# Kernel optimization log

Hardware: AMD Instinct MI355X
Metric: run time of the kernel (lower is better)

The kernel has to match this reference:

```python
import jax, jax.numpy as jnp
import numpy as np

B, C, H, D, HID = 1024, 64, 64, 256, 256

def setup_inputs() -> dict:
    key = jax.random.key(0)
    k1, k2, k3, k4, k5, k6, k7, k8 = jax.random.split(key, 8)
    candidate_news_vector = jax.random.normal(k1, (B, C, D), dtype=jnp.float32)
    clicked_news_vector = jax.random.normal(k2, (B, H, D), dtype=jnp.float32)
    mask_cand = jax.random.randint(k3, (B, C), 0, 2).astype(bool).at[:, 0].set(True)
    mask_hist = jax.random.randint(k4, (B, H), 0, 2).astype(bool).at[:, 0].set(True)
    # nn.Linear default init: U(-1/sqrt(fan_in), 1/sqrt(fan_in))
    s1 = 1.0 / np.sqrt(2 * D)
    s2 = 1.0 / np.sqrt(HID)
    W1 = jax.random.uniform(k5, (HID, 2 * D), minval=-s1, maxval=s1, dtype=jnp.float32)
    b1 = jax.random.uniform(k6, (HID,), minval=-s1, maxval=s1, dtype=jnp.float32)
    W2 = jax.random.uniform(k7, (1, HID), minval=-s2, maxval=s2, dtype=jnp.float32)
    b2 = jax.random.uniform(k8, (1,), minval=-s2, maxval=s2, dtype=jnp.float32)
    return {"candidate_news_vector": candidate_news_vector,
            "clicked_news_vector": clicked_news_vector,
            "mask_cand": mask_cand, "mask_hist": mask_hist,
            "W1": W1, "b1": b1, "W2": W2, "b2": b2}

def reference(candidate_news_vector, clicked_news_vector, mask_cand, mask_hist, W1, b1, W2, b2):
    d = candidate_news_vector.shape[-1]
    w2 = W2[0]                                  # [HID]
    # Two stacked Linears with no nonlinearity collapse exactly:
    # score = (W2 @ W1_c) . cand + (W2 @ W1_h) . hist + (W2 @ b1 + b2)
    v_c = W1[:, :d].T @ w2                      # [D]
    v_h = W1[:, d:].T @ w2                      # [D]
    bias = jnp.dot(w2, b1) + b2[0]
    scores = (jnp.einsum('bcd,d->bc', candidate_news_vector, v_c)[:, :, None]
              + jnp.einsum('bhd,d->bh', clicked_news_vector, v_h)[:, None, :]
              + bias)                           # [B, C, H]
    neg = jnp.finfo(scores.dtype).min
    scores = jnp.where(mask_hist[:, None, :], scores, neg)
    weights = jax.nn.softmax(scores, axis=-1)   # [B, C, H]
    weights = jnp.where(mask_cand[:, :, None], weights, 0.0)
    user_vector = jnp.einsum('bch,bhd->bcd', weights, clicked_news_vector)
    return user_vector
```

## Files before the change

kernel.cpp:

```cpp
#include <hip/hip_runtime.h>
#include <math.h>

#define NB 1024
#define NC 64
#define NH 64
#define ND 256
#define NHID 256

typedef float f4 __attribute__((ext_vector_type(4)));

#define WS_PART_OFF 1024

__device__ __forceinline__ bool read_mask(const void* m, int idx, int mode) {
  if (mode == 2) return ((const float*)m)[idx] != 0.0f;
  if (mode == 1) return ((const unsigned char*)m)[idx] != 0;
  return ((const int*)m)[idx] != 0;
}

__device__ __forceinline__ void detect_mode(const unsigned int* mask_cand,
                                            const unsigned int* mask_hist,
                                            int* dst) {
  int sawf = 0; unsigned int big = 0;
  for (int i = 0; i < 32; ++i) {
    unsigned int a = mask_hist[i], b = mask_cand[i];
    if (a == 0x3f800000u || b == 0x3f800000u) sawf = 1;
    if ((a > 1u && a != 0x3f800000u) || (b > 1u && b != 0x3f800000u)) big = 1;
  }
  *dst = sawf ? 2 : (big ? 1 : 0);
}

__device__ __forceinline__ float dot4(f4 a, f4 b) {
  return fmaf(a.x, b.x, fmaf(a.y, b.y, fmaf(a.z, b.z, a.w * b.w)));
}

#define BFLY(p) { p += __shfl_xor(p, 32); p += __shfl_xor(p, 16); p += __shfl_xor(p, 8); \
                  p += __shfl_xor(p, 4);  p += __shfl_xor(p, 2);  p += __shfl_xor(p, 1); }

__global__ __launch_bounds__(256) void precompute_p1(
    const float* __restrict__ W1, const float* __restrict__ W2,
    float* __restrict__ ws)
{
  const int g = blockIdx.x;
  const int d = threadIdx.x;
  float acc = 0.f;
  #pragma unroll
  for (int jj = 0; jj < 4; ++jj) {
    int j = g * 4 + jj;
    acc = fmaf(W1[(size_t)j * (2 * ND) + ND + d], W2[j], acc);
  }
  ws[WS_PART_OFF + g * ND + d] = acc;
}

__global__ __launch_bounds__(256) void precompute_p2(
    const unsigned int* __restrict__ mask_cand,
    const unsigned int* __restrict__ mask_hist,
    float* __restrict__ ws)
{
  const int d = threadIdx.x;
  float acc = 0.f;
  #pragma unroll 8
  for (int g = 0; g < 64; ++g) acc += ws[WS_PART_OFF + g * ND + d];
  ws[d] = acc;
  if (d == 0) detect_mode(mask_cand, mask_hist, (int*)ws + ND);
}

__global__ __launch_bounds__(1024) void precompute_fallback(
    const float* __restrict__ W1, const float* __restrict__ W2,
    const unsigned int* __restrict__ mask_cand,
    const unsigned int* __restrict__ mask_hist,
    float* __restrict__ ws)
{
  __shared__ float w2_lds[NHID];
  __shared__ float partial[4][ND];
  int t = threadIdx.x;
  if (t < NHID) w2_lds[t] = W2[t];
  __syncthreads();
  int d = t & (ND - 1);
  int g = t >> 8;
  float acc = 0.f;
  #pragma unroll 8
  for (int j = g * 64; j < g * 64 + 64; ++j)
    acc = fmaf(W1[(size_t)j * (2 * ND) + ND + d], w2_lds[j], acc);
  partial[g][d] = acc;
  __syncthreads();
  if (t < ND)
    ws[t] = partial[0][t] + partial[1][t] + partial[2][t] + partial[3][t];
  if (t == 0) detect_mode(mask_cand, mask_hist, (int*)ws + ND);
}

__global__ __launch_bounds__(512, 8) void fused_kernel(
    const float* __restrict__ hist,
    const void* __restrict__ mask_cand_v,
    const void* __restrict__ mask_hist_v,
    const float* __restrict__ ws,
    float* __restrict__ out)
{
  const int b = blockIdx.x, t = threadIdx.x, lane = t & 63, w = t >> 6;
  __shared__ float s_lds[NH];
  __shared__ f4 red[8][64];

  const int mode = ((const int*)ws)[ND];
  const f4* hb4 = reinterpret_cast<const f4*>(hist) + (size_t)b * 4096;
  const f4 vh = reinterpret_cast<const f4*>(ws)[lane];

  bool mc[8];
  #pragma unroll
  for (int j = 0; j < 8; ++j)
    mc[j] = read_mask(mask_cand_v, b * NC + w * 8 + j, mode);

  f4 x0 = hb4[(w * 8 + 0) * 64 + lane], x1 = hb4[(w * 8 + 1) * 64 + lane];
  f4 x2 = hb4[(w * 8 + 2) * 64 + lane], x3 = hb4[(w * 8 + 3) * 64 + lane];
  f4 x4 = hb4[(w * 8 + 4) * 64 + lane], x5 = hb4[(w * 8 + 5) * 64 + lane];
  f4 x6 = hb4[(w * 8 + 6) * 64 + lane], x7 = hb4[(w * 8 + 7) * 64 + lane];

  float p0 = dot4(x0, vh), p1 = dot4(x1, vh), p2 = dot4(x2, vh), p3 = dot4(x3, vh);
  float p4 = dot4(x4, vh), p5 = dot4(x5, vh), p6 = dot4(x6, vh), p7 = dot4(x7, vh);
  BFLY(p0) BFLY(p1) BFLY(p2) BFLY(p3) BFLY(p4) BFLY(p5) BFLY(p6) BFLY(p7)

  if (lane < 8) {
    float v = p0;
    if (lane == 1) v = p1;  if (lane == 2) v = p2;  if (lane == 3) v = p3;
    if (lane == 4) v = p4;  if (lane == 5) v = p5;  if (lane == 6) v = p6;
    if (lane == 7) v = p7;
    int h = w * 8 + lane;
    s_lds[h] = read_mask(mask_hist_v, b * NH + h, mode) ? v : -3.0e38f;
  }
  __syncthreads();

  float wval;
  {
    float s = s_lds[lane];
    float m = s;
    m = fmaxf(m, __shfl_xor(m, 32)); m = fmaxf(m, __shfl_xor(m, 16));
    m = fmaxf(m, __shfl_xor(m, 8));  m = fmaxf(m, __shfl_xor(m, 4));
    m = fmaxf(m, __shfl_xor(m, 2));  m = fmaxf(m, __shfl_xor(m, 1));
    float e = expf(s - m);
    float sum = e;
    BFLY(sum)
    wval = e / sum;
  }

  {
    f4 acc = __shfl(wval, w * 8 + 0) * x0;
    acc += __shfl(wval, w * 8 + 1) * x1;
    acc += __shfl(wval, w * 8 + 2) * x2;
    acc += __shfl(wval, w * 8 + 3) * x3;
    acc += __shfl(wval, w * 8 + 4) * x4;
    acc += __shfl(wval, w * 8 + 5) * x5;
    acc += __shfl(wval, w * 8 + 6) * x6;
    acc += __shfl(wval, w * 8 + 7) * x7;
    red[w][lane] = acc;
  }
  __syncthreads();

  f4 uv = red[0][lane];
  #pragma unroll
  for (int q = 1; q < 8; ++q) uv += red[q][lane];

  f4* ob4 = reinterpret_cast<f4*>(out) + (size_t)b * 4096;
  const f4 zero = {0.f, 0.f, 0.f, 0.f};
  #pragma unroll
  for (int j = 0; j < 8; ++j) {
    int c = w * 8 + j;
    ob4[c * 64 + lane] = mc[j] ? uv : zero;
  }
}

extern "C" void kernel_launch(void* const* d_in, const int* in_sizes, int n_in,
                              void* d_out, int out_size, void* d_ws, size_t ws_size,
                              hipStream_t stream) {
  (void)in_sizes; (void)n_in; (void)out_size;
  const float* hist = (const float*)d_in[1];
  const void*  mask_cand = d_in[2];
  const void*  mask_hist = d_in[3];
  const float* W1 = (const float*)d_in[4];
  const float* W2 = (const float*)d_in[6];
  float* ws = (float*)d_ws;
  float* out = (float*)d_out;

  if (ws_size >= (size_t)(WS_PART_OFF + 64 * ND) * sizeof(float)) {
    precompute_p1<<<64, 256, 0, stream>>>(W1, W2, ws);
    precompute_p2<<<1, 256, 0, stream>>>(
        (const unsigned int*)mask_cand, (const unsigned int*)mask_hist, ws);
  } else {
    precompute_fallback<<<1, 1024, 0, stream>>>(
        W1, W2, (const unsigned int*)mask_cand, (const unsigned int*)mask_hist, ws);
  }
  fused_kernel<<<NB, 512, 0, stream>>>(hist, mask_cand, mask_hist, ws, out);
}
```

Measured before the change: 43.46 us.

## Process two batches per block and prefetch the second batch's history during the first

The fused kernel now handles two batch rows per block, launching half as many blocks. The second row's history tile is loaded while the first row's weighted sum and output write proceed, so memory latency overlaps with compute. This doubles the register footprint, lowers the occupancy hint, and halves the number of blocks available to fill the GPU.

New measurement: 40.34 us. -7.2%, faster.

```diff
diff --git a/kernel.cpp b/kernel.cpp
--- a/kernel.cpp
+++ b/kernel.cpp
@@ -88,81 +88,135 @@
   if (t == 0) detect_mode(mask_cand, mask_hist, (int*)ws + ND);
 }
 
-__global__ __launch_bounds__(512, 8) void fused_kernel(
+__global__ __launch_bounds__(512, 4) void fused2_kernel(
     const float* __restrict__ hist,
     const void* __restrict__ mask_cand_v,
     const void* __restrict__ mask_hist_v,
     const float* __restrict__ ws,
     float* __restrict__ out)
 {
-  const int b = blockIdx.x, t = threadIdx.x, lane = t & 63, w = t >> 6;
-  __shared__ float s_lds[NH];
-  __shared__ f4 red[8][64];
+  const int b0 = blockIdx.x, b1 = blockIdx.x + 512;
+  const int t = threadIdx.x, lane = t & 63, w = t >> 6;
+  __shared__ float s_lds[2][NH];
+  __shared__ f4 red[2][8][64];
 
   const int mode = ((const int*)ws)[ND];
-  const f4* hb4 = reinterpret_cast<const f4*>(hist) + (size_t)b * 4096;
   const f4 vh = reinterpret_cast<const f4*>(ws)[lane];
-
-  bool mc[8];
-  #pragma unroll
-  for (int j = 0; j < 8; ++j)
-    mc[j] = read_mask(mask_cand_v, b * NC + w * 8 + j, mode);
-
-  f4 x0 = hb4[(w * 8 + 0) * 64 + lane], x1 = hb4[(w * 8 + 1) * 64 + lane];
-  f4 x2 = hb4[(w * 8 + 2) * 64 + lane], x3 = hb4[(w * 8 + 3) * 64 + lane];
-  f4 x4 = hb4[(w * 8 + 4) * 64 + lane], x5 = hb4[(w * 8 + 5) * 64 + lane];
-  f4 x6 = hb4[(w * 8 + 6) * 64 + lane], x7 = hb4[(w * 8 + 7) * 64 + lane];
+  const f4* h0 = reinterpret_cast<const f4*>(hist) + (size_t)b0 * 4096;
+  const f4* h1 = reinterpret_cast<const f4*>(hist) + (size_t)b1 * 4096;
+  const f4 zero = {0.f, 0.f, 0.f, 0.f};
+
+  f4 x0 = h0[(w * 8 + 0) * 64 + lane], x1 = h0[(w * 8 + 1) * 64 + lane];
+  f4 x2 = h0[(w * 8 + 2) * 64 + lane], x3 = h0[(w * 8 + 3) * 64 + lane];
+  f4 x4 = h0[(w * 8 + 4) * 64 + lane], x5 = h0[(w * 8 + 5) * 64 + lane];
+  f4 x6 = h0[(w * 8 + 6) * 64 + lane], x7 = h0[(w * 8 + 7) * 64 + lane];
 
   float p0 = dot4(x0, vh), p1 = dot4(x1, vh), p2 = dot4(x2, vh), p3 = dot4(x3, vh);
   float p4 = dot4(x4, vh), p5 = dot4(x5, vh), p6 = dot4(x6, vh), p7 = dot4(x7, vh);
   BFLY(p0) BFLY(p1) BFLY(p2) BFLY(p3) BFLY(p4) BFLY(p5) BFLY(p6) BFLY(p7)
-
   if (lane < 8) {
     float v = p0;
     if (lane == 1) v = p1;  if (lane == 2) v = p2;  if (lane == 3) v = p3;
     if (lane == 4) v = p4;  if (lane == 5) v = p5;  if (lane == 6) v = p6;
     if (lane == 7) v = p7;
     int h = w * 8 + lane;
-    s_lds[h] = read_mask(mask_hist_v, b * NH + h, mode) ? v : -3.0e38f;
-  }
-  __syncthreads();
-
-  float wval;
-  {
-    float s = s_lds[lane];
+    s_lds[0][h] = read_mask(mask_hist_v, b0 * NH + h, mode) ? v : -3.0e38f;
+  }
+  __syncthreads();
+
+  float wval0;
+  {
+    float s = s_lds[0][lane];
     float m = s;
     m = fmaxf(m, __shfl_xor(m, 32)); m = fmaxf(m, __shfl_xor(m, 16));
     m = fmaxf(m, __shfl_xor(m, 8));  m = fmaxf(m, __shfl_xor(m, 4));
     m = fmaxf(m, __shfl_xor(m, 2));  m = fmaxf(m, __shfl_xor(m, 1));
     float e = expf(s - m);
-    float sum = e;
-    BFLY(sum)
-    wval = e / sum;
-  }
-
-  {
-    f4 acc = __shfl(wval, w * 8 + 0) * x0;
-    acc += __shfl(wval, w * 8 + 1) * x1;
-    acc += __shfl(wval, w * 8 + 2) * x2;
-    acc += __shfl(wval, w * 8 + 3) * x3;
-    acc += __shfl(wval, w * 8 + 4) * x4;
-    acc += __shfl(wval, w * 8 + 5) * x5;
-    acc += __shfl(wval, w * 8 + 6) * x6;
-    acc += __shfl(wval, w * 8 + 7) * x7;
-    red[w][lane] = acc;
-  }
-  __syncthreads();
-
-  f4 uv = red[0][lane];
-  #pragma unroll
-  for (int q = 1; q < 8; ++q) uv += red[q][lane];
-
-  f4* ob4 = reinterpret_cast<f4*>(out) + (size_t)b * 4096;
-  const f4 zero = {0.f, 0.f, 0.f, 0.f};
-  #pragma unroll
-  for (int j = 0; j < 8; ++j) {
-    int c = w * 8 + j;
-    ob4[c * 64 + lane] = mc[j] ? uv : zero;
+    float sum = e; BFLY(sum)
+    wval0 = e / sum;
+  }
+
+  {
+    f4 acc = __shfl(wval0, w * 8 + 0) * x0;
+    acc += __shfl(wval0, w * 8 + 1) * x1;
+    acc += __shfl(wval0, w * 8 + 2) * x2;
+    acc += __shfl(wval0, w * 8 + 3) * x3;
+    acc += __shfl(wval0, w * 8 + 4) * x4;
+    acc += __shfl(wval0, w * 8 + 5) * x5;
+    acc += __shfl(wval0, w * 8 + 6) * x6;
+    acc += __shfl(wval0, w * 8 + 7) * x7;
+    red[0][w][lane] = acc;
+  }
+
+  f4 y0 = h1[(w * 8 + 0) * 64 + lane], y1 = h1[(w * 8 + 1) * 64 + lane];
+  f4 y2 = h1[(w * 8 + 2) * 64 + lane], y3 = h1[(w * 8 + 3) * 64 + lane];
+  f4 y4 = h1[(w * 8 + 4) * 64 + lane], y5 = h1[(w * 8 + 5) * 64 + lane];
+  f4 y6 = h1[(w * 8 + 6) * 64 + lane], y7 = h1[(w * 8 + 7) * 64 + lane];
+
+  __syncthreads();
+
+  {
+    f4 uv = red[0][0][lane];
+    #pragma unroll
+    for (int q = 1; q < 8; ++q) uv += red[0][q][lane];
+    f4* ob4 = reinterpret_cast<f4*>(out) + (size_t)b0 * 4096;
+    #pragma unroll
+    for (int j = 0; j < 8; ++j) {
+      int c = w * 8 + j;
+      bool mc = read_mask(mask_cand_v, b0 * NC + c, mode);
+      ob4[c * 64 + lane] = mc ? uv : zero;
+    }
+  }
+
+  float q0 = dot4(y0, vh), q1 = dot4(y1, vh), q2 = dot4(y2, vh), q3 = dot4(y3, vh);
+  float q4 = dot4(y4, vh), q5 = dot4(y5, vh), q6 = dot4(y6, vh), q7 = dot4(y7, vh);
+  BFLY(q0) BFLY(q1) BFLY(q2) BFLY(q3) BFLY(q4) BFLY(q5) BFLY(q6) BFLY(q7)
+  if (lane < 8) {
+    float v = q0;
+    if (lane == 1) v = q1;  if (lane == 2) v = q2;  if (lane == 3) v = q3;
+    if (lane == 4) v = q4;  if (lane == 5) v = q5;  if (lane == 6) v = q6;
+    if (lane == 7) v = q7;
+    int h = w * 8 + lane;
+    s_lds[1][h] = read_mask(mask_hist_v, b1 * NH + h, mode) ? v : -3.0e38f;
+  }
+  __syncthreads();
+
+  float wval1;
+  {
+    float s = s_lds[1][lane];
+    float m = s;
+    m = fmaxf(m, __shfl_xor(m, 32)); m = fmaxf(m, __shfl_xor(m, 16));
+    m = fmaxf(m, __shfl_xor(m, 8));  m = fmaxf(m, __shfl_xor(m, 4));
+    m = fmaxf(m, __shfl_xor(m, 2));  m = fmaxf(m, __shfl_xor(m, 1));
+    float e = expf(s - m);
+    float sum = e; BFLY(sum)
+    wval1 = e / sum;
+  }
+
+  {
+    f4 acc = __shfl(wval1, w * 8 + 0) * y0;
+    acc += __shfl(wval1, w * 8 + 1) * y1;
+    acc += __shfl(wval1, w * 8 + 2) * y2;
+    acc += __shfl(wval1, w * 8 + 3) * y3;
+    acc += __shfl(wval1, w * 8 + 4) * y4;
+    acc += __shfl(wval1, w * 8 + 5) * y5;
+    acc += __shfl(wval1, w * 8 + 6) * y6;
+    acc += __shfl(wval1, w * 8 + 7) * y7;
+    red[1][w][lane] = acc;
+  }
+  __syncthreads();
+
+  {
+    f4 uv = red[1][0][lane];
+    #pragma unroll
+    for (int q = 1; q < 8; ++q) uv += red[1][q][lane];
+    f4* ob4 = reinterpret_cast<f4*>(out) + (size_t)b1 * 4096;
+    #pragma unroll
+    for (int j = 0; j < 8; ++j) {
+      int c = w * 8 + j;
+      bool mc = read_mask(mask_cand_v, b1 * NC + c, mode);
+      ob4[c * 64 + lane] = mc ? uv : zero;
+    }
   }
 }
 
@@ -186,5 +240,5 @@
     precompute_fallback<<<1, 1024, 0, stream>>>(
         W1, W2, (const unsigned int*)mask_cand, (const unsigned int*)mask_hist, ws);
   }
-  fused_kernel<<<NB, 512, 0, stream>>>(hist, mask_cand, mask_hist, ws, out);
-}
+  fused2_kernel<<<NB / 2, 512, 0, stream>>>(hist, mask_cand, mask_hist, ws, out);
+}
```

## Process four batches per block with double-buffered register prefetch of history

Applied to the files above, without the earlier changes.

The fused kernel now handles four batch rows per block, with 256 blocks instead of 1024. It keeps two register sets of history vectors so the next batch's loads are issued while the current batch computes. Mask reads for all four batches are hoisted up front and packed into bitmasks. __syncthreads is replaced by an inline lgkmcnt wait plus s_barrier. This aims to hide memory latency and amortise per-block setup, at the cost of more registers, fewer blocks to spread across CUs, and WAR reuse of the shared buffers across iterations relying on the barriers.

After: 46.08 us. +6.0%, slower.

```diff
diff --git a/kernel.cpp b/kernel.cpp
--- a/kernel.cpp
+++ b/kernel.cpp
@@ -10,6 +10,8 @@
 typedef float f4 __attribute__((ext_vector_type(4)));
 
 #define WS_PART_OFF 1024
+
+#define BAR_LGKM() asm volatile("s_waitcnt lgkmcnt(0)\n\ts_barrier" ::: "memory")
 
 __device__ __forceinline__ bool read_mask(const void* m, int idx, int mode) {
   if (mode == 2) return ((const float*)m)[idx] != 0.0f;
@@ -88,82 +90,111 @@
   if (t == 0) detect_mode(mask_cand, mask_hist, (int*)ws + ND);
 }
 
-__global__ __launch_bounds__(512, 8) void fused_kernel(
+#define LOAD8(R0,R1,R2,R3,R4,R5,R6,R7, BB)                                     \
+  {                                                                            \
+    const f4* hp_ = reinterpret_cast<const f4*>(hist) + (size_t)(BB) * 4096;   \
+    R0 = hp_[(w * 8 + 0) * 64 + lane]; R1 = hp_[(w * 8 + 1) * 64 + lane];      \
+    R2 = hp_[(w * 8 + 2) * 64 + lane]; R3 = hp_[(w * 8 + 3) * 64 + lane];      \
+    R4 = hp_[(w * 8 + 4) * 64 + lane]; R5 = hp_[(w * 8 + 5) * 64 + lane];      \
+    R6 = hp_[(w * 8 + 6) * 64 + lane]; R7 = hp_[(w * 8 + 7) * 64 + lane];      \
+  }
+
+#define PROC(X0,X1,X2,X3,X4,X5,X6,X7, BC, MHV, MCB)                            \
+  {                                                                            \
+    float p0 = dot4(X0, vh), p1 = dot4(X1, vh), p2 = dot4(X2, vh),             \
+          p3 = dot4(X3, vh), p4 = dot4(X4, vh), p5 = dot4(X5, vh),             \
+          p6 = dot4(X6, vh), p7 = dot4(X7, vh);                                \
+    BFLY(p0) BFLY(p1) BFLY(p2) BFLY(p3) BFLY(p4) BFLY(p5) BFLY(p6) BFLY(p7)    \
+    if (lane < 8) {                                                            \
+      float v_ = p0;                                                           \
+      if (lane == 1) v_ = p1;  if (lane == 2) v_ = p2;  if (lane == 3) v_ = p3;\
+      if (lane == 4) v_ = p4;  if (lane == 5) v_ = p5;  if (lane == 6) v_ = p6;\
+      if (lane == 7) v_ = p7;                                                  \
+      s_lds[w * 8 + lane] = (MHV) ? v_ : -3.0e38f;                             \
+    }                                                                          \
+    BAR_LGKM();                                                                \
+    float wval_;                                                               \
+    {                                                                          \
+      float s_ = s_lds[lane];                                                  \
+      float m_ = s_;                                                           \
+      m_ = fmaxf(m_, __shfl_xor(m_, 32)); m_ = fmaxf(m_, __shfl_xor(m_, 16));  \
+      m_ = fmaxf(m_, __shfl_xor(m_, 8));  m_ = fmaxf(m_, __shfl_xor(m_, 4));   \
+      m_ = fmaxf(m_, __shfl_xor(m_, 2));  m_ = fmaxf(m_, __shfl_xor(m_, 1));   \
+      float e_ = expf(s_ - m_);                                                \
+      float sum_ = e_; BFLY(sum_)                                              \
+      wval_ = e_ / sum_;                                                       \
+    }                                                                          \
+    {                                                                          \
+      f4 acc_ = __shfl(wval_, w * 8 + 0) * X0;                                 \
+      acc_ += __shfl(wval_, w * 8 + 1) * X1;                                   \
+      acc_ += __shfl(wval_, w * 8 + 2) * X2;                                   \
+      acc_ += __shfl(wval_, w * 8 + 3) * X3;                                   \
+      acc_ += __shfl(wval_, w * 8 + 4) * X4;                                   \
+      acc_ += __shfl(wval_, w * 8 + 5) * X5;                                   \
+      acc_ += __shfl(wval_, w * 8 + 6) * X6;                                   \
+      acc_ += __shfl(wval_, w * 8 + 7) * X7;                                   \
+      red[w][lane] = acc_;                                                     \
+    }                                                                          \
+    BAR_LGKM();                                                                \
+    {                                                                          \
+      f4 uv_ = red[0][lane];                                                   \
+      _Pragma("unroll")                                                        \
+      for (int q_ = 1; q_ < 8; ++q_) uv_ += red[q_][lane];                     \
+      f4* ob4_ = reinterpret_cast<f4*>(out) + (size_t)(BC) * 4096;             \
+      _Pragma("unroll")                                                        \
+      for (int j_ = 0; j_ < 8; ++j_) {                                         \
+        int c_ = w * 8 + j_;                                                   \
+        ob4_[c_ * 64 + lane] = (((MCB) >> j_) & 1u) ? uv_ : zero;              \
+      }                                                                        \
+    }                                                                          \
+  }
+
+__global__ __launch_bounds__(512, 4) void fused4_kernel(
     const float* __restrict__ hist,
     const void* __restrict__ mask_cand_v,
     const void* __restrict__ mask_hist_v,
     const float* __restrict__ ws,
     float* __restrict__ out)
 {
-  const int b = blockIdx.x, t = threadIdx.x, lane = t & 63, w = t >> 6;
+  const int t = threadIdx.x, lane = t & 63, w = t >> 6;
+  const int b0 = blockIdx.x * 4;
   __shared__ float s_lds[NH];
   __shared__ f4 red[8][64];
 
   const int mode = ((const int*)ws)[ND];
-  const f4* hb4 = reinterpret_cast<const f4*>(hist) + (size_t)b * 4096;
   const f4 vh = reinterpret_cast<const f4*>(ws)[lane];
-
-  bool mc[8];
-  #pragma unroll
-  for (int j = 0; j < 8; ++j)
-    mc[j] = read_mask(mask_cand_v, b * NC + w * 8 + j, mode);
-
-  f4 x0 = hb4[(w * 8 + 0) * 64 + lane], x1 = hb4[(w * 8 + 1) * 64 + lane];
-  f4 x2 = hb4[(w * 8 + 2) * 64 + lane], x3 = hb4[(w * 8 + 3) * 64 + lane];
-  f4 x4 = hb4[(w * 8 + 4) * 64 + lane], x5 = hb4[(w * 8 + 5) * 64 + lane];
-  f4 x6 = hb4[(w * 8 + 6) * 64 + lane], x7 = hb4[(w * 8 + 7) * 64 + lane];
-
-  float p0 = dot4(x0, vh), p1 = dot4(x1, vh), p2 = dot4(x2, vh), p3 = dot4(x3, vh);
-  float p4 = dot4(x4, vh), p5 = dot4(x5, vh), p6 = dot4(x6, vh), p7 = dot4(x7, vh);
-  BFLY(p0) BFLY(p1) BFLY(p2) BFLY(p3) BFLY(p4) BFLY(p5) BFLY(p6) BFLY(p7)
-
+  const f4 zero = {0.f, 0.f, 0.f, 0.f};
+
+  f4 x0, x1, x2, x3, x4, x5, x6, x7;
+  f4 y0, y1, y2, y3, y4, y5, y6, y7;
+
+  LOAD8(x0,x1,x2,x3,x4,x5,x6,x7, b0 + 0);
+  LOAD8(y0,y1,y2,y3,y4,y5,y6,y7, b0 + 1);
+
+  int mhv0 = 0, mhv1 = 0, mhv2 = 0, mhv3 = 0;
   if (lane < 8) {
-    float v = p0;
-    if (lane == 1) v = p1;  if (lane == 2) v = p2;  if (lane == 3) v = p3;
-    if (lane == 4) v = p4;  if (lane == 5) v = p5;  if (lane == 6) v = p6;
-    if (lane == 7) v = p7;
     int h = w * 8 + lane;
-    s_lds[h] = read_mask(mask_hist_v, b * NH + h, mode) ? v : -3.0e38f;
-  }
-  __syncthreads();
-
-  float wval;
-  {
-    float s = s_lds[lane];
-    float m = s;
-    m = fmaxf(m, __shfl_xor(m, 32)); m = fmaxf(m, __shfl_xor(m, 16));
-    m = fmaxf(m, __shfl_xor(m, 8));  m = fmaxf(m, __shfl_xor(m, 4));
-    m = fmaxf(m, __shfl_xor(m, 2));  m = fmaxf(m, __shfl_xor(m, 1));
-    float e = expf(s - m);
-    float sum = e;
-    BFLY(sum)
-    wval = e / sum;
-  }
-
-  {
-    f4 acc = __shfl(wval, w * 8 + 0) * x0;
-    acc += __shfl(wval, w * 8 + 1) * x1;
-    acc += __shfl(wval, w * 8 + 2) * x2;
-    acc += __shfl(wval, w * 8 + 3) * x3;
-    acc += __shfl(wval, w * 8 + 4) * x4;
-    acc += __shfl(wval, w * 8 + 5) * x5;
-    acc += __shfl(wval, w * 8 + 6) * x6;
-    acc += __shfl(wval, w * 8 + 7) * x7;
-    red[w][lane] = acc;
-  }
-  __syncthreads();
-
-  f4 uv = red[0][lane];
-  #pragma unroll
-  for (int q = 1; q < 8; ++q) uv += red[q][lane];
-
-  f4* ob4 = reinterpret_cast<f4*>(out) + (size_t)b * 4096;
-  const f4 zero = {0.f, 0.f, 0.f, 0.f};
+    mhv0 = read_mask(mask_hist_v, (b0 + 0) * NH + h, mode);
+    mhv1 = read_mask(mask_hist_v, (b0 + 1) * NH + h, mode);
+    mhv2 = read_mask(mask_hist_v, (b0 + 2) * NH + h, mode);
+    mhv3 = read_mask(mask_hist_v, (b0 + 3) * NH + h, mode);
+  }
+  unsigned int mcb0 = 0, mcb1 = 0, mcb2 = 0, mcb3 = 0;
   #pragma unroll
   for (int j = 0; j < 8; ++j) {
     int c = w * 8 + j;
-    ob4[c * 64 + lane] = mc[j] ? uv : zero;
-  }
+    mcb0 |= (unsigned int)read_mask(mask_cand_v, (b0 + 0) * NC + c, mode) << j;
+    mcb1 |= (unsigned int)read_mask(mask_cand_v, (b0 + 1) * NC + c, mode) << j;
+    mcb2 |= (unsigned int)read_mask(mask_cand_v, (b0 + 2) * NC + c, mode) << j;
+    mcb3 |= (unsigned int)read_mask(mask_cand_v, (b0 + 3) * NC + c, mode) << j;
+  }
+
+  PROC(x0,x1,x2,x3,x4,x5,x6,x7, b0 + 0, mhv0, mcb0);
+  LOAD8(x0,x1,x2,x3,x4,x5,x6,x7, b0 + 2);
+  PROC(y0,y1,y2,y3,y4,y5,y6,y7, b0 + 1, mhv1, mcb1);
+  LOAD8(y0,y1,y2,y3,y4,y5,y6,y7, b0 + 3);
+  PROC(x0,x1,x2,x3,x4,x5,x6,x7, b0 + 2, mhv2, mcb2);
+  PROC(y0,y1,y2,y3,y4,y5,y6,y7, b0 + 3, mhv3, mcb3);
 }
 
 extern "C" void kernel_launch(void* const* d_in, const int* in_sizes, int n_in,
@@ -186,5 +217,5 @@
     precompute_fallback<<<1, 1024, 0, stream>>>(
         W1, W2, (const unsigned int*)mask_cand, (const unsigned int*)mask_hist, ws);
   }
-  fused_kernel<<<NB, 512, 0, stream>>>(hist, mask_cand, mask_hist, ws, out);
-}
+  fused4_kernel<<<NB / 4, 512, 0, stream>>>(hist, mask_cand, mask_hist, ws, out);
+}
```

## Process each batch row in one wavefront with online softmax and double-buffered loads

Applied to the files above, without the earlier changes.

Each 64-lane wavefront now handles a whole batch row and streams the 64 history vectors in blocks of 8. It keeps a running max and sum (online softmax) and double-buffers the register loads, which removes the LDS exchanges and the two block-wide barriers. Masks are packed into 64-bit ballots instead of being read per element. The cost is much less parallelism per row: 256 blocks of 4 waves instead of 1024 blocks of 8 waves, so each wave carries a longer serial chain of loads and 64 output stores.

Measured after the change: 40.00 us. -8.0%, faster.

```diff
diff --git a/kernel.cpp b/kernel.cpp
--- a/kernel.cpp
+++ b/kernel.cpp
@@ -88,82 +88,87 @@
   if (t == 0) detect_mode(mask_cand, mask_hist, (int*)ws + ND);
 }
 
-__global__ __launch_bounds__(512, 8) void fused_kernel(
+#define LOADB(R0,R1,R2,R3,R4,R5,R6,R7, H0)                                     \
+  R0 = hp4[((H0) + 0) * 64 + lane]; R1 = hp4[((H0) + 1) * 64 + lane];          \
+  R2 = hp4[((H0) + 2) * 64 + lane]; R3 = hp4[((H0) + 3) * 64 + lane];          \
+  R4 = hp4[((H0) + 4) * 64 + lane]; R5 = hp4[((H0) + 5) * 64 + lane];          \
+  R6 = hp4[((H0) + 6) * 64 + lane]; R7 = hp4[((H0) + 7) * 64 + lane];
+
+#define PROCB(R0,R1,R2,R3,R4,R5,R6,R7, H0)                                     \
+  {                                                                            \
+    float p0 = dot4(R0, vhq), p1 = dot4(R1, vhq), p2 = dot4(R2, vhq),          \
+          p3 = dot4(R3, vhq), p4 = dot4(R4, vhq), p5 = dot4(R5, vhq),          \
+          p6 = dot4(R6, vhq), p7 = dot4(R7, vhq);                              \
+    BFLY(p0) BFLY(p1) BFLY(p2) BFLY(p3) BFLY(p4) BFLY(p5) BFLY(p6) BFLY(p7)    \
+    p0 = ((mh >> ((H0) + 0)) & 1) ? p0 : -3.0e38f;                             \
+    p1 = ((mh >> ((H0) + 1)) & 1) ? p1 : -3.0e38f;                             \
+    p2 = ((mh >> ((H0) + 2)) & 1) ? p2 : -3.0e38f;                             \
+    p3 = ((mh >> ((H0) + 3)) & 1) ? p3 : -3.0e38f;                             \
+    p4 = ((mh >> ((H0) + 4)) & 1) ? p4 : -3.0e38f;                             \
+    p5 = ((mh >> ((H0) + 5)) & 1) ? p5 : -3.0e38f;                             \
+    p6 = ((mh >> ((H0) + 6)) & 1) ? p6 : -3.0e38f;                             \
+    p7 = ((mh >> ((H0) + 7)) & 1) ? p7 : -3.0e38f;                             \
+    float pm = fmaxf(fmaxf(fmaxf(p0, p1), fmaxf(p2, p3)),                      \
+                     fmaxf(fmaxf(p4, p5), fmaxf(p6, p7)));                     \
+    float mn = fmaxf(mrun, pm);                                                \
+    float sc = expf(mrun - mn);                                                \
+    float e0 = expf(p0 - mn), e1 = expf(p1 - mn), e2 = expf(p2 - mn),          \
+          e3 = expf(p3 - mn), e4 = expf(p4 - mn), e5 = expf(p5 - mn),          \
+          e6 = expf(p6 - mn), e7 = expf(p7 - mn);                              \
+    srun = srun * sc + ((e0 + e1) + (e2 + e3)) + ((e4 + e5) + (e6 + e7));      \
+    acc = acc * sc;                                                            \
+    acc += e0 * R0; acc += e1 * R1; acc += e2 * R2; acc += e3 * R3;            \
+    acc += e4 * R4; acc += e5 * R5; acc += e6 * R6; acc += e7 * R7;            \
+    mrun = mn;                                                                 \
+  }
+
+__global__ __launch_bounds__(256) void flash_kernel(
     const float* __restrict__ hist,
     const void* __restrict__ mask_cand_v,
     const void* __restrict__ mask_hist_v,
     const float* __restrict__ ws,
     float* __restrict__ out)
 {
-  const int b = blockIdx.x, t = threadIdx.x, lane = t & 63, w = t >> 6;
-  __shared__ float s_lds[NH];
-  __shared__ f4 red[8][64];
+  const int t = threadIdx.x, lane = t & 63, w = t >> 6;
+  const int b = blockIdx.x * 4 + w;
 
   const int mode = ((const int*)ws)[ND];
-  const f4* hb4 = reinterpret_cast<const f4*>(hist) + (size_t)b * 4096;
-  const f4 vh = reinterpret_cast<const f4*>(ws)[lane];
+  const f4* hp4 = reinterpret_cast<const f4*>(hist) + (size_t)b * 4096;
+  const f4 vhq = reinterpret_cast<const f4*>(ws)[lane];
 
-  bool mc[8];
+  const unsigned long long mh =
+      __ballot(read_mask(mask_hist_v, b * NH + lane, mode));
+  const unsigned long long mc =
+      __ballot(read_mask(mask_cand_v, b * NC + lane, mode));
+
+  float mrun = -3.0e38f, srun = 0.f;
+  f4 acc = {0.f, 0.f, 0.f, 0.f};
+  f4 x0, x1, x2, x3, x4, x5, x6, x7;
+  f4 y0, y1, y2, y3, y4, y5, y6, y7;
+
+  LOADB(x0,x1,x2,x3,x4,x5,x6,x7, 0)
+  LOADB(y0,y1,y2,y3,y4,y5,y6,y7, 8)
+  PROCB(x0,x1,x2,x3,x4,x5,x6,x7, 0)
+  LOADB(x0,x1,x2,x3,x4,x5,x6,x7, 16)
+  PROCB(y0,y1,y2,y3,y4,y5,y6,y7, 8)
+  LOADB(y0,y1,y2,y3,y4,y5,y6,y7, 24)
+  PROCB(x0,x1,x2,x3,x4,x5,x6,x7, 16)
+  LOADB(x0,x1,x2,x3,x4,x5,x6,x7, 32)
+  PROCB(y0,y1,y2,y3,y4,y5,y6,y7, 24)
+  LOADB(y0,y1,y2,y3,y4,y5,y6,y7, 40)
+  PROCB(x0,x1,x2,x3,x4,x5,x6,x7, 32)
+  LOADB(x0,x1,x2,x3,x4,x5,x6,x7, 48)
+  PROCB(y0,y1,y2,y3,y4,y5,y6,y7, 40)
+  LOADB(y0,y1,y2,y3,y4,y5,y6,y7, 56)
+  PROCB(x0,x1,x2,x3,x4,x5,x6,x7, 48)
+  PROCB(y0,y1,y2,y3,y4,y5,y6,y7, 56)
+
+  const f4 uv = acc * (1.0f / srun);
+  const f4 zero = {0.f, 0.f, 0.f, 0.f};
+  f4* ob4 = reinterpret_cast<f4*>(out) + (size_t)b * 4096;
   #pragma unroll
-  for (int j = 0; j < 8; ++j)
-    mc[j] = read_mask(mask_cand_v, b * NC + w * 8 + j, mode);
-
-  f4 x0 = hb4[(w * 8 + 0) * 64 + lane], x1 = hb4[(w * 8 + 1) * 64 + lane];
-  f4 x2 = hb4[(w * 8 + 2) * 64 + lane], x3 = hb4[(w * 8 + 3) * 64 + lane];
-  f4 x4 = hb4[(w * 8 + 4) * 64 + lane], x5 = hb4[(w * 8 + 5) * 64 + lane];
-  f4 x6 = hb4[(w * 8 + 6) * 64 + lane], x7 = hb4[(w * 8 + 7) * 64 + lane];
-
-  float p0 = dot4(x0, vh), p1 = dot4(x1, vh), p2 = dot4(x2, vh), p3 = dot4(x3, vh);
-  float p4 = dot4(x4, vh), p5 = dot4(x5, vh), p6 = dot4(x6, vh), p7 = dot4(x7, vh);
-  BFLY(p0) BFLY(p1) BFLY(p2) BFLY(p3) BFLY(p4) BFLY(p5) BFLY(p6) BFLY(p7)
-
-  if (lane < 8) {
-    float v = p0;
-    if (lane == 1) v = p1;  if (lane == 2) v = p2;  if (lane == 3) v = p3;
-    if (lane == 4) v = p4;  if (lane == 5) v = p5;  if (lane == 6) v = p6;
-    if (lane == 7) v = p7;
-    int h = w * 8 + lane;
-    s_lds[h] = read_mask(mask_hist_v, b * NH + h, mode) ? v : -3.0e38f;
-  }
-  __syncthreads();
-
-  float wval;
-  {
-    float s = s_lds[lane];
-    float m = s;
-    m = fmaxf(m, __shfl_xor(m, 32)); m = fmaxf(m, __shfl_xor(m, 16));
-    m = fmaxf(m, __shfl_xor(m, 8));  m = fmaxf(m, __shfl_xor(m, 4));
-    m = fmaxf(m, __shfl_xor(m, 2));  m = fmaxf(m, __shfl_xor(m, 1));
-    float e = expf(s - m);
-    float sum = e;
-    BFLY(sum)
-    wval = e / sum;
-  }
-
-  {
-    f4 acc = __shfl(wval, w * 8 + 0) * x0;
-    acc += __shfl(wval, w * 8 + 1) * x1;
-    acc += __shfl(wval, w * 8 + 2) * x2;
-    acc += __shfl(wval, w * 8 + 3) * x3;
-    acc += __shfl(wval, w * 8 + 4) * x4;
-    acc += __shfl(wval, w * 8 + 5) * x5;
-    acc += __shfl(wval, w * 8 + 6) * x6;
-    acc += __shfl(wval, w * 8 + 7) * x7;
-    red[w][lane] = acc;
-  }
-  __syncthreads();
-
-  f4 uv = red[0][lane];
-  #pragma unroll
-  for (int q = 1; q < 8; ++q) uv += red[q][lane];
-
-  f4* ob4 = reinterpret_cast<f4*>(out) + (size_t)b * 4096;
-  const f4 zero = {0.f, 0.f, 0.f, 0.f};
-  #pragma unroll
-  for (int j = 0; j < 8; ++j) {
-    int c = w * 8 + j;
-    ob4[c * 64 + lane] = mc[j] ? uv : zero;
-  }
+  for (int c = 0; c < 64; ++c)
+    ob4[c * 64 + lane] = ((mc >> c) & 1ull) ? uv : zero;
 }
 
 extern "C" void kernel_launch(void* const* d_in, const int* in_sizes, int n_in,
@@ -186,5 +191,5 @@
     precompute_fallback<<<1, 1024, 0, stream>>>(
         W1, W2, (const unsigned int*)mask_cand, (const unsigned int*)mask_hist, ws);
   }
-  fused_kernel<<<NB, 512, 0, stream>>>(hist, mask_cand, mask_hist, ws, out);
+  flash_kernel<<<NB / 4, 256, 0, stream>>>(hist, mask_cand, mask_hist, ws, out);
 }
```
